# Optimization experiments

Hardware: AMD Instinct MI355X
Metric: run time of the kernel (lower is better)

## Reference

```python
import jax, jax.numpy as jnp
import numpy as np

B, T, D = 32, 256, 512
DUR_MAX = 12            # durations drawn from [0, 12)
MAX_FRAMES = T * (DUR_MAX - 1)  # static upper bound on expanded length (2816)
PAD_VALUE = 0.0


def setup_inputs() -> dict:
    key = jax.random.key(0)
    k1, k2 = jax.random.split(key)
    xs = jax.random.normal(k1, (B, T, D), dtype=jnp.float32)
    ds = jax.random.randint(k2, (B, T), 0, DUR_MAX, dtype=jnp.int64)
    return {"xs": xs, "ds": ds}


def _length_regulate(xs, ds):
    # Cumsum-based expand: frame f of batch b copies token t where
    # cumsum(ds)[b, t-1] <= f < cumsum(ds)[b, t]  (tokens with d==0 are skipped
    # automatically since they occupy zero frames).
    cs = jnp.cumsum(ds, axis=1)                      # [B, T]
    total = cs[:, -1]                                # [B] total frames per batch
    frame_ids = jnp.arange(MAX_FRAMES)               # [F]
    # token index for each output frame (searchsorted right => first t with cs[t] > f)
    tok = jax.vmap(lambda c: jnp.searchsorted(c, frame_ids, side="right"))(cs)  # [B, F]
    tok = jnp.clip(tok, 0, T - 1)
    out = jnp.take_along_axis(xs, tok[:, :, None], axis=1)  # [B, F, D]
    valid = frame_ids[None, :] < total[:, None]              # [B, F]
    return jnp.where(valid[:, :, None], out, jnp.asarray(PAD_VALUE, xs.dtype))


def reference(xs, ds):
    return _length_regulate(xs, ds)
```

## Files before the change

kernel.cpp:

```cpp
#include <hip/hip_runtime.h>

#define BB 32
#define TT 256
#define DD 512
#define DUR_MAX_ 12
#define MAX_FRAMES_ (TT * (DUR_MAX_ - 1))
#define FRAMES_PER_BLOCK 64
#define D4 (DD / 4)
#define BLOCK_THREADS 256

typedef float f32x4 __attribute__((ext_vector_type(4)));

__global__ __launch_bounds__(BLOCK_THREADS)
void LengthRegulator_20332375179470_kernel(const float* __restrict__ xs,
                                           const int* __restrict__ ds,
                                           float* __restrict__ out)
{
    __shared__ int s_cs[TT];
    __shared__ int s_wsum[BLOCK_THREADS / 64];
    __shared__ int s_tok[FRAMES_PER_BLOCK];

    const int b    = blockIdx.y;
    const int f0   = blockIdx.x * FRAMES_PER_BLOCK;
    const int tid  = threadIdx.x;
    const int lane = tid & 63;
    const int wid  = tid >> 6;

    int v = ds[b * TT + tid];
    #pragma unroll
    for (int off = 1; off < 64; off <<= 1) {
        int n = __shfl_up(v, off, 64);
        if (lane >= off) v += n;
    }
    if (lane == 63) s_wsum[wid] = v;
    __syncthreads();
    int woff = 0;
    #pragma unroll
    for (int w = 0; w < BLOCK_THREADS / 64; ++w)
        if (w < wid) woff += s_wsum[w];
    s_cs[tid] = v + woff;
    __syncthreads();
    const int total = s_cs[TT - 1];

    if (tid < FRAMES_PER_BLOCK) {
        const int f = f0 + tid;
        if (f < total) {
            int lo = 0, hi = TT;
            while (lo < hi) {
                int mid = (lo + hi) >> 1;
                if (s_cs[mid] <= f) lo = mid + 1; else hi = mid;
            }
            if (lo > TT - 1) lo = TT - 1;
            s_tok[tid] = lo;
        } else {
            s_tok[tid] = -1;
        }
    }
    __syncthreads();

    const f32x4* xs4  = (const f32x4*)(xs + (size_t)b * TT * DD);
    f32x4*       out4 = (f32x4*)(out + ((size_t)b * MAX_FRAMES_ + f0) * DD);

    #pragma unroll
    for (int i = 0; i < (FRAMES_PER_BLOCK * D4) / BLOCK_THREADS; ++i) {
        const int l   = i * BLOCK_THREADS + tid;
        const int fl  = l >> 7;
        const int d4  = l & (D4 - 1);
        const int tok = s_tok[fl];
        f32x4 val = (f32x4)(0.f);
        if (tok >= 0) val = xs4[tok * D4 + d4];
        out4[l] = val;
    }
}

extern "C" void kernel_launch(void* const* d_in, const int* in_sizes, int n_in,
                              void* d_out, int out_size, void* d_ws, size_t ws_size,
                              hipStream_t stream) {
    const float* xs = (const float*)d_in[0];
    const int*   ds = (const int*)d_in[1];
    float*       out = (float*)d_out;

    dim3 grid(MAX_FRAMES_ / FRAMES_PER_BLOCK, BB);
    LengthRegulator_20332375179470_kernel<<<grid, BLOCK_THREADS, 0, stream>>>(xs, ds, out);
}
```

Before: 32.61 us.

## Scatter token rows to frames instead of per-frame binary search gather

Replaces the per-frame gather, which binary-searched the cumsum for every frame, with token-centric blocks. Each wave loads one token row once into registers and writes it to all of its duration frames. Separate pad blocks zero only the frames beyond the total length, and fully valid pad blocks exit early. This cuts the binary-search work and the repeated reads of xs. In exchange, the work per wave is uneven, since durations vary from 0 to 11 frames per token, and the grid launches more blocks, each of which recomputes the cumsum.

```diff
diff --git a/kernel.cpp b/kernel.cpp
--- a/kernel.cpp
+++ b/kernel.cpp
@@ -5,9 +5,12 @@
 #define DD 512
 #define DUR_MAX_ 12
 #define MAX_FRAMES_ (TT * (DUR_MAX_ - 1))
-#define FRAMES_PER_BLOCK 64
 #define D4 (DD / 4)
 #define BLOCK_THREADS 256
+#define TOKENS_PER_BLOCK 4
+#define TOKEN_BLOCKS (TT / TOKENS_PER_BLOCK)
+#define PAD_FPB 64
+#define PAD_BLOCKS (MAX_FRAMES_ / PAD_FPB)
 
 typedef float f32x4 __attribute__((ext_vector_type(4)));
 
@@ -18,10 +21,8 @@
 {
     __shared__ int s_cs[TT];
     __shared__ int s_wsum[BLOCK_THREADS / 64];
-    __shared__ int s_tok[FRAMES_PER_BLOCK];
 
     const int b    = blockIdx.y;
-    const int f0   = blockIdx.x * FRAMES_PER_BLOCK;
     const int tid  = threadIdx.x;
     const int lane = tid & 63;
     const int wid  = tid >> 6;
@@ -42,34 +43,31 @@
     __syncthreads();
     const int total = s_cs[TT - 1];
 
-    if (tid < FRAMES_PER_BLOCK) {
-        const int f = f0 + tid;
-        if (f < total) {
-            int lo = 0, hi = TT;
-            while (lo < hi) {
-                int mid = (lo + hi) >> 1;
-                if (s_cs[mid] <= f) lo = mid + 1; else hi = mid;
+    if (blockIdx.x < TOKEN_BLOCKS) {
+        const int t     = blockIdx.x * TOKENS_PER_BLOCK + wid;
+        const int end   = s_cs[t];
+        const int start = (t > 0) ? s_cs[t - 1] : 0;
+        if (end > start) {
+            const f32x4* row = (const f32x4*)(xs + ((size_t)b * TT + t) * DD);
+            const f32x4 v0 = row[lane];
+            const f32x4 v1 = row[64 + lane];
+            f32x4* ob = (f32x4*)(out + (size_t)b * MAX_FRAMES_ * DD);
+            for (int r = start; r < end; ++r) {
+                f32x4* o = ob + (size_t)r * D4;
+                o[lane]      = v0;
+                o[64 + lane] = v1;
             }
-            if (lo > TT - 1) lo = TT - 1;
-            s_tok[tid] = lo;
-        } else {
-            s_tok[tid] = -1;
         }
-    }
-    __syncthreads();
-
-    const f32x4* xs4  = (const f32x4*)(xs + (size_t)b * TT * DD);
-    f32x4*       out4 = (f32x4*)(out + ((size_t)b * MAX_FRAMES_ + f0) * DD);
-
-    #pragma unroll
-    for (int i = 0; i < (FRAMES_PER_BLOCK * D4) / BLOCK_THREADS; ++i) {
-        const int l   = i * BLOCK_THREADS + tid;
-        const int fl  = l >> 7;
-        const int d4  = l & (D4 - 1);
-        const int tok = s_tok[fl];
-        f32x4 val = (f32x4)(0.f);
-        if (tok >= 0) val = xs4[tok * D4 + d4];
-        out4[l] = val;
+    } else {
+        const int f0 = (blockIdx.x - TOKEN_BLOCKS) * PAD_FPB;
+        if (f0 + PAD_FPB <= total) return;
+        f32x4* ob = (f32x4*)(out + ((size_t)b * MAX_FRAMES_ + f0) * DD);
+        #pragma unroll
+        for (int i = 0; i < (PAD_FPB * D4) / BLOCK_THREADS; ++i) {
+            const int l  = i * BLOCK_THREADS + tid;
+            const int fl = l >> 7;
+            if (f0 + fl >= total) ob[l] = (f32x4)(0.f);
+        }
     }
 }
 
@@ -80,6 +78,6 @@
     const int*   ds = (const int*)d_in[1];
     float*       out = (float*)d_out;
 
-    dim3 grid(MAX_FRAMES_ / FRAMES_PER_BLOCK, BB);
+    dim3 grid(TOKEN_BLOCKS + PAD_BLOCKS, BB);
     LengthRegulator_20332375179470_kernel<<<grid, BLOCK_THREADS, 0, stream>>>(xs, ds, out);
 }
```

Result: slower. 33.49 us (+2.7%).
